# Kernel optimization log

Hardware: AMD Instinct MI355X
Metric: run time of the kernel (lower is better)

## Reference

```python
import jax, jax.numpy as jnp
import numpy as np

# --- MLA config (matches init_kwargs) ---
DIM = 2048
H = 16
KV_RANK = 512
Q_RANK = 1536
ROPE = 64          # qk_rope_head_dim (even)
NOPE = 128         # qk_nope_head_dim
VD = 128           # v_head_dim
THETA = 500000.0
EPS = 1e-6
B, T = 1, 2048
QK_HEAD = NOPE + ROPE  # logits use nope + rope dims


def _rmsnorm(x, w):
    # x float32; RMS over last dim, no mean subtraction
    rms = jax.lax.rsqrt(jnp.mean(x * x, axis=-1, keepdims=True) + EPS)
    return (x * rms) * w


def _rope_tables(t):
    inv_freq = 1.0 / (THETA ** (jnp.arange(0, ROPE, 2, dtype=jnp.float32) / ROPE))  # (ROPE/2,)
    pos = jnp.arange(t, dtype=jnp.float32)
    angles = jnp.outer(pos, inv_freq)  # (T, ROPE/2)
    return jnp.cos(angles), jnp.sin(angles)


def _apply_rope(x, cos, sin):
    # x: (B, T, Hx, D) with adjacent-pair rotation; cos/sin: (T, D/2)
    b, t, h, d = x.shape
    xp = x.reshape(b, t, h, d // 2, 2)
    even, odd = xp[..., 0], xp[..., 1]
    c = cos.reshape(1, t, 1, d // 2)
    s = sin.reshape(1, t, 1, d // 2)
    out = jnp.stack((even * c - odd * s, odd * c + even * s), axis=-1)
    return out.reshape(b, t, h, d)


def setup_inputs() -> dict:
    key = jax.random.key(0)
    ks = jax.random.split(key, 7)
    s = 0.02
    x = jax.random.normal(ks[0], (B, T, DIM), dtype=jnp.float32)
    w_q_down = jax.random.normal(ks[1], (Q_RANK, DIM), dtype=jnp.float32) * s
    q_norm_w = jnp.ones((Q_RANK,), dtype=jnp.float32)
    w_q_up = jax.random.normal(ks[2], (H * (NOPE + ROPE), Q_RANK), dtype=jnp.float32) * s
    w_kv_down = jax.random.normal(ks[3], (KV_RANK + ROPE, DIM), dtype=jnp.float32) * s
    kv_norm_w = jnp.ones((KV_RANK,), dtype=jnp.float32)
    w_kv_up = jax.random.normal(ks[4], (H * (NOPE + VD), KV_RANK), dtype=jnp.float32) * s
    w_o = jax.random.normal(ks[5], (DIM, H * VD), dtype=jnp.float32) * s
    return {"x": x, "w_q_down": w_q_down, "q_norm_w": q_norm_w, "w_q_up": w_q_up,
            "w_kv_down": w_kv_down, "kv_norm_w": kv_norm_w, "w_kv_up": w_kv_up, "w_o": w_o}


def reference(x, w_q_down, q_norm_w, w_q_up, w_kv_down, kv_norm_w, w_kv_up, w_o):
    b, t, _ = x.shape
    # Query path: down-proj -> RMSNorm -> up-proj, split nope/rope
    c_q = _rmsnorm(x @ w_q_down.T, q_norm_w)                       # (B,T,Q_RANK)
    q = (c_q @ w_q_up.T).reshape(b, t, H, NOPE + ROPE)
    q_nope, q_rope = q[..., :NOPE], q[..., NOPE:]
    # KV path: down-proj -> split latent c_kv and shared rope key
    kv = x @ w_kv_down.T                                           # (B,T,KV_RANK+ROPE)
    c_kv = kv[..., :KV_RANK]
    k_rope_raw = kv[..., KV_RANK:].reshape(b, t, 1, ROPE)
    # RoPE (adjacent-pair), start_pos=0
    cos, sin = _rope_tables(t)
    q_rope = _apply_rope(q_rope, cos, sin)
    k_rope = _apply_rope(k_rope_raw, cos, sin)                     # (B,T,1,ROPE) shared head
    # Reconstruct k_nope and v from normalized latent
    kv_up = (_rmsnorm(c_kv, kv_norm_w) @ w_kv_up.T).reshape(b, t, H, NOPE + VD)
    k_nope, v = kv_up[..., :NOPE], kv_up[..., NOPE:]
    # Assemble full q/k (rope key broadcast across heads)
    q_full = jnp.concatenate((q_nope, q_rope), axis=-1)            # (B,T,H,QK_HEAD)
    k_full = jnp.concatenate((k_nope, jnp.broadcast_to(k_rope, (b, t, H, ROPE))), axis=-1)
    # Causal attention
    scale = 1.0 / np.sqrt(QK_HEAD)
    scores = jnp.einsum('bqhd,bkhd->bhqk', q_full, k_full) * scale  # (B,H,T,T)
    causal = jnp.tril(jnp.ones((t, t), dtype=bool))
    scores = jnp.where(causal[None, None], scores, -jnp.inf)
    attn = jax.nn.softmax(scores, axis=-1)
    out = jnp.einsum('bhqk,bkhd->bqhd', attn, v).reshape(b, t, H * VD)
    return out @ w_o.T                                             # (B,T,DIM)
```

## Files before the change

kernel.cpp:

```cpp
#include <hip/hip_runtime.h>
#include <hip/hip_bf16.h>

typedef short short8 __attribute__((ext_vector_type(8)));
typedef float f32x4 __attribute__((ext_vector_type(4)));

#define DIM 2048
#define NH 16
#define KV_RANK 512
#define Q_RANK 1536
#define ROPE_D 64
#define NOPE 128
#define VD 128
#define TT 2048
#define QKH 192
#define QD (NH * QKH)
#define KVUP_D (NH * (NOPE + VD))
#define WDN 2176

__device__ inline unsigned short f2bf(float f) {
  __hip_bfloat16 h = __float2bfloat16(f);
  union { __hip_bfloat16 h; unsigned short u; } cv; cv.h = h; return cv.u;
}
__device__ inline float bf2f(unsigned short u) {
  union { unsigned int i; float f; } cv; cv.i = ((unsigned int)u) << 16; return cv.f;
}
__device__ inline void gload_lds16(const void* g, void* l) {
  __builtin_amdgcn_global_load_lds(
      (const __attribute__((address_space(1))) void*)g,
      (__attribute__((address_space(3))) void*)l, 16, 0, 0);
}

__global__ __launch_bounds__(256) void convert_all(
    const float* __restrict__ x, const float* __restrict__ wqd,
    const float* __restrict__ wkvd, const float* __restrict__ wqu,
    const float* __restrict__ wkvu, const float* __restrict__ wo,
    unsigned short* __restrict__ xb, unsigned short* __restrict__ wdb,
    unsigned short* __restrict__ wqub, unsigned short* __restrict__ wkvub,
    unsigned short* __restrict__ wob) {
  int i = blockIdx.x * 256 + threadIdx.x;
  const int n0 = TT * DIM / 4;
  const int n1 = WDN * 2048 / 4;
  const int n2 = QD * Q_RANK / 4;
  const int n3 = KVUP_D * KV_RANK / 4;
  const int n4 = DIM * DIM / 4;
  float4 v;
  unsigned short* dst;
  if (i < n0) { v = reinterpret_cast<const float4*>(x)[i]; dst = xb; }
  else if ((i -= n0) < n1) {
    int row = i >> 9, c4 = i & 511;
    if (row < 1536)      v = reinterpret_cast<const float4*>(wqd)[row * 512 + c4];
    else if (row < 2112) v = reinterpret_cast<const float4*>(wkvd)[(row - 1536) * 512 + c4];
    else                 v = make_float4(0.f, 0.f, 0.f, 0.f);
    dst = wdb;
  }
  else if ((i -= n1) < n2) { v = reinterpret_cast<const float4*>(wqu)[i]; dst = wqub; }
  else if ((i -= n2) < n3) { v = reinterpret_cast<const float4*>(wkvu)[i]; dst = wkvub; }
  else if ((i -= n3) < n4) { v = reinterpret_cast<const float4*>(wo)[i]; dst = wob; }
  else return;
  ushort4 o;
  o.x = f2bf(v.x); o.y = f2bf(v.y); o.z = f2bf(v.z); o.w = f2bf(v.w);
  reinterpret_cast<ushort4*>(dst)[i] = o;
}

__device__ __forceinline__ void gemm_core(const unsigned short* __restrict__ A,
                                          const unsigned short* __restrict__ W,
                                          unsigned short* As, unsigned short* Bs,
                                          int K, int lda, int ldb,
                                          int bm, int bn, int tid,
                                          f32x4 (&acc)[4][4]) {
  const int lane = tid & 63, wave = tid >> 6;
  const int wm = (wave >> 1) * 64, wn = (wave & 1) * 64;
  const int fr = lane & 15, fg = lane >> 4;
  const int sr = lane >> 3, scb = (lane & 7) ^ sr;
  const int r0 = wave * 32;

  const unsigned short* Ag = A + (size_t)(bm + r0 + sr) * lda + scb * 8;
  const unsigned short* Wg = W + (size_t)(bn + r0 + sr) * ldb + scb * 8;
  const int nt = K >> 6;

#pragma unroll
  for (int i = 0; i < 4; ++i) {
    gload_lds16(Ag + (size_t)(i * 8) * lda, As + r0 * 64 + i * 512);
    gload_lds16(Wg + (size_t)(i * 8) * ldb, Bs + r0 * 64 + i * 512);
  }
  int cur = 0;
  for (int t = 0; t < nt; ++t) {
    if (t + 1 < nt) {
      const int nb = cur ^ 1;
      const int ko = (t + 1) * 64;
#pragma unroll
      for (int i = 0; i < 4; ++i) {
        gload_lds16(Ag + ko + (size_t)(i * 8) * lda, As + nb * 8192 + r0 * 64 + i * 512);
        gload_lds16(Wg + ko + (size_t)(i * 8) * ldb, Bs + nb * 8192 + r0 * 64 + i * 512);
      }
      asm volatile("s_waitcnt vmcnt(8)" ::: "memory");
    } else {
      asm volatile("s_waitcnt vmcnt(0)" ::: "memory");
    }
    __builtin_amdgcn_s_barrier();
    asm volatile("" ::: "memory");
    const unsigned short* Ac = As + cur * 8192;
    const unsigned short* Bc = Bs + cur * 8192;
    __builtin_amdgcn_s_setprio(1);
#pragma unroll
    for (int kk = 0; kk < 2; ++kk) {
      short8 a[4], b[4];
#pragma unroll
      for (int i = 0; i < 4; ++i) {
        int ra = wm + i * 16 + fr;
        a[i] = *reinterpret_cast<const short8*>(&Ac[ra * 64 + (((kk * 4 + fg) ^ (ra & 7)) * 8)]);
        int rb = wn + i * 16 + fr;
        b[i] = *reinterpret_cast<const short8*>(&Bc[rb * 64 + (((kk * 4 + fg) ^ (rb & 7)) * 8)]);
      }
#pragma unroll
      for (int i = 0; i < 4; ++i)
#pragma unroll
        for (int j = 0; j < 4; ++j)
          acc[i][j] = __builtin_amdgcn_mfma_f32_16x16x32_bf16(a[i], b[j], acc[i][j], 0, 0, 0);
    }
    __builtin_amdgcn_s_setprio(0);
    asm volatile("" ::: "memory");
    __builtin_amdgcn_s_barrier();
    cur ^= 1;
  }
}

__global__ __launch_bounds__(256) void gemm_fast(const unsigned short* __restrict__ A,
                                                 const unsigned short* __restrict__ W,
                                                 float* __restrict__ Cf,
                                                 unsigned short* __restrict__ Cb,
                                                 int K, int lda, int ldb, int ldc) {
  __shared__ __align__(16) unsigned short As[2 * 128 * 64];
  __shared__ __align__(16) unsigned short Bs[2 * 128 * 64];
  const int tid = threadIdx.x;
  const int bm = blockIdx.y * 128, bn = blockIdx.x * 128;
  const int lane = tid & 63, wave = tid >> 6;
  const int wm = (wave >> 1) * 64, wn = (wave & 1) * 64;
  const int fr = lane & 15, fg = lane >> 4;

  f32x4 acc[4][4] = {};
  gemm_core(A, W, As, Bs, K, lda, ldb, bm, bn, tid, acc);

  if (Cb) {
#pragma unroll
    for (int i = 0; i < 4; ++i) {
      int row0 = bm + wm + i * 16 + fg * 4;
#pragma unroll
      for (int j = 0; j < 4; ++j) {
        int col = bn + wn + j * 16 + fr;
#pragma unroll
        for (int r = 0; r < 4; ++r)
          Cb[(size_t)(row0 + r) * ldc + col] = f2bf(acc[i][j][r]);
      }
    }
  } else {
#pragma unroll
    for (int i = 0; i < 4; ++i) {
      int row0 = bm + wm + i * 16 + fg * 4;
#pragma unroll
      for (int j = 0; j < 4; ++j) {
        int col = bn + wn + j * 16 + fr;
#pragma unroll
        for (int r = 0; r < 4; ++r)
          Cf[(size_t)(row0 + r) * ldc + col] = acc[i][j][r];
      }
    }
  }
}

__global__ __launch_bounds__(256) void gemm_dual(
    const unsigned short* __restrict__ A1, const unsigned short* __restrict__ W1,
    unsigned short* __restrict__ C1,
    const unsigned short* __restrict__ A2, const unsigned short* __restrict__ W2,
    unsigned short* __restrict__ kbuf, unsigned short* __restrict__ vt) {
  __shared__ __align__(16) unsigned short As[2 * 128 * 64];
  __shared__ __align__(16) unsigned short Bs[2 * 128 * 64];
  const int tid = threadIdx.x;
  const int bx = blockIdx.x;
  const unsigned short *A, *W;
  int K, lda, bm, bn;
  const bool isq = (bx < 384);
  if (isq) {
    A = A1; W = W1; K = Q_RANK; lda = Q_RANK;
    bn = (bx % 24) * 128; bm = (bx / 24) * 128;
  } else {
    int b2 = bx - 384;
    A = A2; W = W2; K = KV_RANK; lda = KV_RANK;
    bn = (b2 & 31) * 128; bm = (b2 >> 5) * 128;
  }
  const int lane = tid & 63, wave = tid >> 6;
  const int wm = (wave >> 1) * 64, wn = (wave & 1) * 64;
  const int fr = lane & 15, fg = lane >> 4;

  f32x4 acc[4][4] = {};
  gemm_core(A, W, As, Bs, K, lda, lda, bm, bn, tid, acc);

  if (isq) {
#pragma unroll
    for (int i = 0; i < 4; ++i) {
      int row0 = bm + wm + i * 16 + fg * 4;
#pragma unroll
      for (int j = 0; j < 4; ++j) {
        int col = bn + wn + j * 16 + fr;
#pragma unroll
        for (int r = 0; r < 4; ++r)
          C1[(size_t)(row0 + r) * QD + col] = f2bf(acc[i][j][r]);
      }
    }
  } else {
#pragma unroll
    for (int i = 0; i < 4; ++i) {
      int row0 = bm + wm + i * 16 + fg * 4;
#pragma unroll
      for (int j = 0; j < 4; ++j) {
        int col = bn + wn + j * 16 + fr;
        int hh = col >> 8, cc = col & 255;
        if (cc < 128) {
#pragma unroll
          for (int r = 0; r < 4; ++r)
            kbuf[((size_t)hh * TT + row0 + r) * QKH + cc] = f2bf(acc[i][j][r]);
        } else {
          ushort4 w4;
          w4.x = f2bf(acc[i][j][0]); w4.y = f2bf(acc[i][j][1]);
          w4.z = f2bf(acc[i][j][2]); w4.w = f2bf(acc[i][j][3]);
          *reinterpret_cast<ushort4*>(vt + (size_t)(hh * VD + cc - 128) * TT + row0) = w4;
        }
      }
    }
  }
}

__global__ __launch_bounds__(256) void rmsnorm_bf16(const unsigned short* __restrict__ in,
                                                    int instride, int inoff,
                                                    const float* __restrict__ w,
                                                    unsigned short* __restrict__ out,
                                                    int outstride, int cols) {
  const int row = blockIdx.x, tid = threadIdx.x;
  const unsigned short* x = in + (size_t)row * instride + inoff;
  const int nch = cols >> 3;
  float ss = 0.f;
  for (int cb = tid; cb < nch; cb += 256) {
    short8 v = *reinterpret_cast<const short8*>(x + cb * 8);
#pragma unroll
    for (int e = 0; e < 8; ++e) { float f = bf2f((unsigned short)v[e]); ss += f * f; }
  }
  __shared__ float red[256];
  red[tid] = ss; __syncthreads();
  for (int off = 128; off > 0; off >>= 1) {
    if (tid < off) red[tid] += red[tid + off];
    __syncthreads();
  }
  float r = rsqrtf(red[0] / (float)cols + 1e-6f);
  for (int cb = tid; cb < nch; cb += 256) {
    short8 v = *reinterpret_cast<const short8*>(x + cb * 8);
    ushort4 o0, o1;
    o0.x = f2bf(bf2f((unsigned short)v[0]) * r * w[cb * 8 + 0]);
    o0.y = f2bf(bf2f((unsigned short)v[1]) * r * w[cb * 8 + 1]);
    o0.z = f2bf(bf2f((unsigned short)v[2]) * r * w[cb * 8 + 2]);
    o0.w = f2bf(bf2f((unsigned short)v[3]) * r * w[cb * 8 + 3]);
    o1.x = f2bf(bf2f((unsigned short)v[4]) * r * w[cb * 8 + 4]);
    o1.y = f2bf(bf2f((unsigned short)v[5]) * r * w[cb * 8 + 5]);
    o1.z = f2bf(bf2f((unsigned short)v[6]) * r * w[cb * 8 + 6]);
    o1.w = f2bf(bf2f((unsigned short)v[7]) * r * w[cb * 8 + 7]);
    *reinterpret_cast<ushort4*>(out + (size_t)row * outstride + cb * 8) = o0;
    *reinterpret_cast<ushort4*>(out + (size_t)row * outstride + cb * 8 + 4) = o1;
  }
}

__global__ __launch_bounds__(256) void rope_kernel(unsigned short* __restrict__ qb,
                                                   const unsigned short* __restrict__ cqkv,
                                                   unsigned short* __restrict__ kbuf) {
  const int t = blockIdx.x, tid = threadIdx.x;
  unsigned short* qrow = qb + (size_t)t * QD;
  for (int p = tid; p < NH * 32 + 32; p += 256) {
    int j = (p < NH * 32) ? (p & 31) : (p - NH * 32);
    float inv = powf(500000.0f, -(float)(2 * j) * (1.0f / 64.0f));
    float ang = (float)t * inv;
    float sv, cv;
    sincosf(ang, &sv, &cv);
    if (p < NH * 32) {
      int h = p >> 5;
      unsigned short* b = qrow + h * QKH + NOPE + 2 * j;
      float e = bf2f(b[0]), o = bf2f(b[1]);
      b[0] = f2bf(e * cv - o * sv);
      b[1] = f2bf(o * cv + e * sv);
    } else {
      const unsigned short* b = cqkv + (size_t)t * WDN + 2048 + 2 * j;
      float e = bf2f(b[0]), o = bf2f(b[1]);
      unsigned short re = f2bf(e * cv - o * sv);
      unsigned short ro = f2bf(o * cv + e * sv);
#pragma unroll
      for (int hh = 0; hh < NH; ++hh) {
        kbuf[((size_t)hh * TT + t) * QKH + NOPE + 2 * j]     = re;
        kbuf[((size_t)hh * TT + t) * QKH + NOPE + 2 * j + 1] = ro;
      }
    }
  }
}

__global__ __launch_bounds__(256, 2) void attn_part(
    const unsigned short* __restrict__ qb,
    const unsigned short* __restrict__ kbuf,
    const unsigned short* __restrict__ vtb,
    unsigned short* __restrict__ Opart,
    float* __restrict__ ml)
{
  const int b = blockIdx.x;
  const int h = b & 15;
  const int w = b >> 4;
  int qt, c;
  if (w < 16)      { qt = 15 - (w >> 2); c = w & 3; }
  else if (w < 28) { int v = w - 16; qt = 11 - v / 3; c = v % 3; }
  else if (w < 36) { int v = w - 28; qt = 7 - ((w - 28) >> 1); c = v & 1; }
  else             { qt = 3 - (w - 36); c = 0; }
  const int t0 = qt * 128;
  const int ktlo = c * 8;
  const int kthi = min(c * 8 + 8, 2 * qt + 2);
  const int tid = threadIdx.x;
  const int lane = tid & 63, wv = tid >> 6;
  const int fr = lane & 15, fg = lane >> 4;

  __shared__ __align__(16) unsigned short KVl[2560 * 8];
  __shared__ __align__(16) unsigned short Ps[4][16 * 64];
  unsigned short* Kl = KVl;
  unsigned short* Vt = KVl + 12288;

  short8 qf[2][6];
#pragma unroll
  for (int s = 0; s < 2; ++s) {
    const unsigned short* qrow = qb + (size_t)(t0 + wv * 32 + s * 16 + fr) * QD + h * QKH;
#pragma unroll
    for (int kc = 0; kc < 6; ++kc)
      qf[s][kc] = *reinterpret_cast<const short8*>(qrow + kc * 32 + fg * 8);
  }

  f32x4 o[2][8] = {};
  float m2[2] = {-1e30f, -1e30f};
  float l2[2] = {0.f, 0.f};
  const float scale = 0.0721687836487032f;
  const unsigned short* kb = kbuf + (size_t)h * TT * QKH;
  const unsigned short* vb = vtb + (size_t)h * VD * TT;

  for (int kt = ktlo; kt < kthi; ++kt) {
    const int kt0 = kt * 64;
#pragma unroll
    for (int i = 0; i < 6; ++i) {
      int u = tid + i * 256;
      int row = u / 24, cb = u - (u / 24) * 24;
      int cbs = cb ^ (row & 7);
      gload_lds16(kb + (size_t)(kt0 + row) * QKH + cbs * 8, Kl + u * 8);
    }
#pragma unroll
    for (int i = 0; i < 4; ++i) {
      int u = tid + i * 256;
      int d = u >> 3, cb = u & 7;
      int cbs = cb ^ (d & 7);
      gload_lds16(vb + (size_t)d * TT + kt0 + cbs * 8, Vt + u * 8);
    }
    asm volatile("s_waitcnt vmcnt(0)" ::: "memory");
    __syncthreads();

    f32x4 sA[2][4] = {};
    __builtin_amdgcn_s_setprio(1);
#pragma unroll
    for (int kc = 0; kc < 6; ++kc) {
#pragma unroll
      for (int kr = 0; kr < 4; ++kr) {
        int row = kr * 16 + fr;
        short8 kf = *reinterpret_cast<const short8*>(
            &Kl[row * QKH + (((kc * 4 + fg) ^ (row & 7)) * 8)]);
        sA[0][kr] = __builtin_amdgcn_mfma_f32_16x16x32_bf16(kf, qf[0][kc], sA[0][kr], 0, 0, 0);
        sA[1][kr] = __builtin_amdgcn_mfma_f32_16x16x32_bf16(kf, qf[1][kc], sA[1][kr], 0, 0, 0);
      }
    }
    __builtin_amdgcn_s_setprio(0);

    const bool diag = (kt0 + 64 > t0);
#pragma unroll
    for (int s = 0; s < 2; ++s) {
      const int qg = t0 + wv * 32 + s * 16 + fr;
      float mx = -1e30f;
#pragma unroll
      for (int kr = 0; kr < 4; ++kr)
#pragma unroll
        for (int r = 0; r < 4; ++r) {
          float svv = sA[s][kr][r] * scale;
          if (diag && (kt0 + kr * 16 + fg * 4 + r) > qg) svv = -1e30f;
          sA[s][kr][r] = svv;
          mx = fmaxf(mx, svv);
        }
      mx = fmaxf(mx, __shfl_xor(mx, 16));
      mx = fmaxf(mx, __shfl_xor(mx, 32));
      float mn = fmaxf(m2[s], mx);
      float corr = __expf(m2[s] - mn);
      m2[s] = mn;
      float ssum = 0.f;
#pragma unroll
      for (int kr = 0; kr < 4; ++kr) {
        ushort4 pk;
        float p0 = __expf(sA[s][kr][0] - mn);
        float p1 = __expf(sA[s][kr][1] - mn);
        float p2 = __expf(sA[s][kr][2] - mn);
        float p3 = __expf(sA[s][kr][3] - mn);
        ssum += p0 + p1 + p2 + p3;
        pk.x = f2bf(p0); pk.y = f2bf(p1); pk.z = f2bf(p2); pk.w = f2bf(p3);
        *reinterpret_cast<ushort4*>(
            &Ps[wv][fr * 64 + (((kr * 2 + (fg >> 1)) ^ (fr & 7)) * 8) + (fg & 1) * 4]) = pk;
      }
      ssum += __shfl_xor(ssum, 16);
      ssum += __shfl_xor(ssum, 32);
      l2[s] = l2[s] * corr + ssum;
      if (__any(corr != 1.0f)) {
        float c0 = __shfl(corr, fg * 4 + 0);
        float c1 = __shfl(corr, fg * 4 + 1);
        float c2 = __shfl(corr, fg * 4 + 2);
        float c3 = __shfl(corr, fg * 4 + 3);
#pragma unroll
        for (int dj = 0; dj < 8; ++dj) {
          o[s][dj][0] *= c0; o[s][dj][1] *= c1;
          o[s][dj][2] *= c2; o[s][dj][3] *= c3;
        }
      }
      __builtin_amdgcn_s_setprio(1);
#pragma unroll
      for (int kk = 0; kk < 2; ++kk) {
        short8 pa = *reinterpret_cast<const short8*>(
            &Ps[wv][fr * 64 + (((kk * 4 + fg) ^ (fr & 7)) * 8)]);
#pragma unroll
        for (int dj = 0; dj < 8; ++dj) {
          int dv = dj * 16 + fr;
          short8 bv = *reinterpret_cast<const short8*>(
              &Vt[dv * 64 + (((kk * 4 + fg) ^ (dv & 7)) * 8)]);
          o[s][dj] = __builtin_amdgcn_mfma_f32_16x16x32_bf16(pa, bv, o[s][dj], 0, 0, 0);
        }
      }
      __builtin_amdgcn_s_setprio(0);
    }
    __syncthreads();
  }

  const int slot = (h * 16 + qt) * 4 + c;
#pragma unroll
  for (int s = 0; s < 2; ++s) {
#pragma unroll
    for (int r = 0; r < 4; ++r) {
      int row = wv * 32 + s * 16 + fg * 4 + r;
      unsigned short* orow = Opart + ((size_t)slot * 128 + row) * 128;
#pragma unroll
      for (int dj = 0; dj < 8; ++dj)
        orow[dj * 16 + fr] = f2bf(o[s][dj][r]);
    }
    if (fg == 0) {
      int row = wv * 32 + s * 16 + fr;
      ml[((size_t)slot * 128 + row) * 2]     = m2[s];
      ml[((size_t)slot * 128 + row) * 2 + 1] = l2[s];
    }
  }
}

__global__ __launch_bounds__(256) void attn_combine(
    const unsigned short* __restrict__ Opart, const float* __restrict__ ml,
    unsigned short* __restrict__ out) {
  const int bid = blockIdx.x;
  const int h = bid >> 5;
  const int qt = (bid >> 1) & 15;
  const int rh = bid & 1;
  const int nch = qt / 4 + 1;
  const int tid = threadIdx.x;
  const int row = rh * 64 + (tid >> 2), dg = tid & 3;
  const int base = (h * 16 + qt) * 4;
  float mm[4], ll[4];
  float M = -1e30f;
#pragma unroll
  for (int cc = 0; cc < 4; ++cc) {
    if (cc < nch) {
      mm[cc] = ml[((size_t)(base + cc) * 128 + row) * 2];
      ll[cc] = ml[((size_t)(base + cc) * 128 + row) * 2 + 1];
      M = fmaxf(M, mm[cc]);
    } else { mm[cc] = -1e30f; ll[cc] = 0.f; }
  }
  float L = 0.f;
#pragma unroll
  for (int cc = 0; cc < 4; ++cc) {
    mm[cc] = __expf(mm[cc] - M);
    L += ll[cc] * mm[cc];
  }
  float acc[32] = {};
#pragma unroll
  for (int cc = 0; cc < 4; ++cc) {
    if (cc < nch) {
      const unsigned short* op = Opart + ((size_t)(base + cc) * 128 + row) * 128 + dg * 32;
      float sc = mm[cc];
#pragma unroll
      for (int e8 = 0; e8 < 4; ++e8) {
        short8 v = *reinterpret_cast<const short8*>(op + e8 * 8);
#pragma unroll
        for (int e = 0; e < 8; ++e) acc[e8 * 8 + e] += bf2f((unsigned short)v[e]) * sc;
      }
    }
  }
  float linv = 1.0f / L;
  unsigned short* dst = out + (size_t)(qt * 128 + row) * DIM + h * VD + dg * 32;
#pragma unroll
  for (int e4 = 0; e4 < 8; ++e4) {
    ushort4 w4;
    w4.x = f2bf(acc[e4 * 4 + 0] * linv);
    w4.y = f2bf(acc[e4 * 4 + 1] * linv);
    w4.z = f2bf(acc[e4 * 4 + 2] * linv);
    w4.w = f2bf(acc[e4 * 4 + 3] * linv);
    *reinterpret_cast<ushort4*>(dst + e4 * 4) = w4;
  }
}

extern "C" void kernel_launch(void* const* d_in, const int* in_sizes, int n_in,
                              void* d_out, int out_size, void* d_ws, size_t ws_size,
                              hipStream_t stream) {
  const float* x        = (const float*)d_in[0];
  const float* w_q_down = (const float*)d_in[1];
  const float* q_norm_w = (const float*)d_in[2];
  const float* w_q_up   = (const float*)d_in[3];
  const float* w_kv_down= (const float*)d_in[4];
  const float* kv_norm_w= (const float*)d_in[5];
  const float* w_kv_up  = (const float*)d_in[6];
  const float* w_o      = (const float*)d_in[7];
  float* outp = (float*)d_out;

  char* ws = (char*)d_ws;
  size_t off = 0;
  auto alloc = [&](size_t bytes) {
    void* p = ws + off;
    off += (bytes + 255) & ~(size_t)255;
    return p;
  };
  unsigned short* x_bf     = (unsigned short*)alloc((size_t)TT * DIM * 2);
  unsigned short* wdown_bf = (unsigned short*)alloc((size_t)WDN * DIM * 2);
  unsigned short* wqu_bf   = (unsigned short*)alloc((size_t)QD * Q_RANK * 2);
  unsigned short* wkvu_bf  = (unsigned short*)alloc((size_t)KVUP_D * KV_RANK * 2);
  unsigned short* wo_bf    = (unsigned short*)alloc((size_t)DIM * DIM * 2);
  unsigned short* cqkv_bf  = (unsigned short*)alloc((size_t)TT * WDN * 2);
  unsigned short* cq_bf    = (unsigned short*)alloc((size_t)TT * Q_RANK * 2);
  unsigned short* ckv_bf   = (unsigned short*)alloc((size_t)TT * KV_RANK * 2);
  unsigned short* qb_bf    = (unsigned short*)alloc((size_t)TT * QD * 2);
  unsigned short* kbuf     = (unsigned short*)alloc((size_t)NH * TT * QKH * 2);
  unsigned short* vtb      = (unsigned short*)alloc((size_t)NH * VD * TT * 2);
  unsigned short* Opart    = (unsigned short*)alloc((size_t)1024 * 128 * 128 * 2);
  float*          mlbuf    = (float*)alloc((size_t)1024 * 128 * 2 * 4);
  unsigned short* attn_bf  = x_bf;

  {
    int total = TT * DIM / 4 + WDN * 2048 / 4 + QD * Q_RANK / 4 +
                KVUP_D * KV_RANK / 4 + DIM * DIM / 4;
    convert_all<<<dim3((total + 255) / 256), dim3(256), 0, stream>>>(
        x, w_q_down, w_kv_down, w_q_up, w_kv_up, w_o,
        x_bf, wdown_bf, wqu_bf, wkvu_bf, wo_bf);
  }

  dim3 blk(256);
  gemm_fast<<<dim3(WDN / 128, TT / 128), blk, 0, stream>>>(
      x_bf, wdown_bf, nullptr, cqkv_bf, DIM, DIM, DIM, WDN);
  rmsnorm_bf16<<<dim3(TT), blk, 0, stream>>>(cqkv_bf, WDN, 0, q_norm_w, cq_bf, Q_RANK, Q_RANK);
  rmsnorm_bf16<<<dim3(TT), blk, 0, stream>>>(cqkv_bf, WDN, Q_RANK, kv_norm_w, ckv_bf, KV_RANK, KV_RANK);
  gemm_dual<<<dim3(896), blk, 0, stream>>>(cq_bf, wqu_bf, qb_bf,
                                           ckv_bf, wkvu_bf, kbuf, vtb);
  rope_kernel<<<dim3(TT), blk, 0, stream>>>(qb_bf, cqkv_bf, kbuf);
  attn_part<<<dim3(640), blk, 0, stream>>>(qb_bf, kbuf, vtb, Opart, mlbuf);
  attn_combine<<<dim3(512), blk, 0, stream>>>(Opart, mlbuf, attn_bf);
  gemm_fast<<<dim3(DIM / 128, TT / 128), blk, 0, stream>>>(
      attn_bf, wo_bf, outp, nullptr, DIM, DIM, DIM, DIM);
}
```

Baseline: 217.9 us.

## Double-buffer K/V tiles in attention with smaller 32-key steps

Splits the K/V tile into 32-key chunks and double-buffers them in LDS, so the global-to-LDS load of the next chunk is issued before computing on the current one, with partial vmcnt waits. The PV product now shares each V fragment across both query subtiles, and the P staging buffer uses a padded layout instead of an XOR swizzle. The aim is to hide global load latency behind MFMA work, at the cost of more loop iterations, more barriers per key, and a possible LDS bank-conflict change from the padded V layout.

After: 227.9 us. 4.6% more time.

```diff
diff --git a/kernel.cpp b/kernel.cpp
--- a/kernel.cpp
+++ b/kernel.cpp
@@ -311,19 +311,38 @@
   int qt, c;
   if (w < 16)      { qt = 15 - (w >> 2); c = w & 3; }
   else if (w < 28) { int v = w - 16; qt = 11 - v / 3; c = v % 3; }
-  else if (w < 36) { int v = w - 28; qt = 7 - ((w - 28) >> 1); c = v & 1; }
+  else if (w < 36) { qt = 7 - ((w - 28) >> 1); c = (w - 28) & 1; }
   else             { qt = 3 - (w - 36); c = 0; }
   const int t0 = qt * 128;
-  const int ktlo = c * 8;
-  const int kthi = min(c * 8 + 8, 2 * qt + 2);
+  const int ktlo = c * 16;
+  const int kthi = min(c * 16 + 16, 4 * qt + 4);
   const int tid = threadIdx.x;
   const int lane = tid & 63, wv = tid >> 6;
   const int fr = lane & 15, fg = lane >> 4;
 
-  __shared__ __align__(16) unsigned short KVl[2560 * 8];
-  __shared__ __align__(16) unsigned short Ps[4][16 * 64];
-  unsigned short* Kl = KVl;
-  unsigned short* Vt = KVl + 12288;
+  __shared__ __align__(16) unsigned short KV[2][12288];
+  __shared__ __align__(16) unsigned short Ps[4][2][16 * 40];
+
+  const unsigned short* kb = kbuf + (size_t)h * TT * QKH;
+  const unsigned short* vb = vtb + (size_t)h * VD * TT;
+
+  auto STAGE = [&](int bi, int kt) {
+    const int kt0s = kt * 32;
+#pragma unroll
+    for (int i = 0; i < 3; ++i) {
+      int u = tid + i * 256;
+      int row = u / 24, cb = u - (u / 24) * 24;
+      gload_lds16(kb + (size_t)(kt0s + row) * QKH + ((cb ^ (row & 7)) * 8),
+                  &KV[bi][u * 8]);
+    }
+#pragma unroll
+    for (int i = 0; i < 3; ++i) {
+      int u = tid + i * 256;
+      int d = u / 6, cb = u - (u / 6) * 6;
+      int cbs = (cb < 4) ? cb : 0;
+      gload_lds16(vb + (size_t)d * TT + kt0s + cbs * 8, &KV[bi][6144 + u * 8]);
+    }
+  };
 
   short8 qf[2][6];
 #pragma unroll
@@ -333,55 +352,51 @@
     for (int kc = 0; kc < 6; ++kc)
       qf[s][kc] = *reinterpret_cast<const short8*>(qrow + kc * 32 + fg * 8);
   }
+  asm volatile("s_waitcnt vmcnt(0)" ::: "memory");
+
+  STAGE(0, ktlo);
 
   f32x4 o[2][8] = {};
   float m2[2] = {-1e30f, -1e30f};
   float l2[2] = {0.f, 0.f};
   const float scale = 0.0721687836487032f;
-  const unsigned short* kb = kbuf + (size_t)h * TT * QKH;
-  const unsigned short* vb = vtb + (size_t)h * VD * TT;
-
+
+  int buf = 0;
   for (int kt = ktlo; kt < kthi; ++kt) {
-    const int kt0 = kt * 64;
-#pragma unroll
-    for (int i = 0; i < 6; ++i) {
-      int u = tid + i * 256;
-      int row = u / 24, cb = u - (u / 24) * 24;
-      int cbs = cb ^ (row & 7);
-      gload_lds16(kb + (size_t)(kt0 + row) * QKH + cbs * 8, Kl + u * 8);
-    }
-#pragma unroll
-    for (int i = 0; i < 4; ++i) {
-      int u = tid + i * 256;
-      int d = u >> 3, cb = u & 7;
-      int cbs = cb ^ (d & 7);
-      gload_lds16(vb + (size_t)d * TT + kt0 + cbs * 8, Vt + u * 8);
-    }
-    asm volatile("s_waitcnt vmcnt(0)" ::: "memory");
-    __syncthreads();
-
-    f32x4 sA[2][4] = {};
+    const int kt0 = kt * 32;
+    if (kt + 1 < kthi) {
+      STAGE(buf ^ 1, kt + 1);
+      asm volatile("s_waitcnt vmcnt(6)" ::: "memory");
+    } else {
+      asm volatile("s_waitcnt vmcnt(0)" ::: "memory");
+    }
+    __builtin_amdgcn_s_barrier();
+    asm volatile("" ::: "memory");
+    const unsigned short* Kb = KV[buf];
+    const unsigned short* Vt = KV[buf] + 6144;
+
+    f32x4 sA[2][2] = {};
     __builtin_amdgcn_s_setprio(1);
 #pragma unroll
     for (int kc = 0; kc < 6; ++kc) {
 #pragma unroll
-      for (int kr = 0; kr < 4; ++kr) {
+      for (int kr = 0; kr < 2; ++kr) {
         int row = kr * 16 + fr;
         short8 kf = *reinterpret_cast<const short8*>(
-            &Kl[row * QKH + (((kc * 4 + fg) ^ (row & 7)) * 8)]);
+            &Kb[row * QKH + (((kc * 4 + fg) ^ (row & 7)) * 8)]);
         sA[0][kr] = __builtin_amdgcn_mfma_f32_16x16x32_bf16(kf, qf[0][kc], sA[0][kr], 0, 0, 0);
         sA[1][kr] = __builtin_amdgcn_mfma_f32_16x16x32_bf16(kf, qf[1][kc], sA[1][kr], 0, 0, 0);
       }
     }
     __builtin_amdgcn_s_setprio(0);
 
-    const bool diag = (kt0 + 64 > t0);
+    const bool diag = (kt0 + 32 > t0);
 #pragma unroll
     for (int s = 0; s < 2; ++s) {
       const int qg = t0 + wv * 32 + s * 16 + fr;
       float mx = -1e30f;
 #pragma unroll
-      for (int kr = 0; kr < 4; ++kr)
+      for (int kr = 0; kr < 2; ++kr)
 #pragma unroll
         for (int r = 0; r < 4; ++r) {
           float svv = sA[s][kr][r] * scale;
@@ -396,16 +411,15 @@
       m2[s] = mn;
       float ssum = 0.f;
 #pragma unroll
-      for (int kr = 0; kr < 4; ++kr) {
-        ushort4 pk;
+      for (int kr = 0; kr < 2; ++kr) {
         float p0 = __expf(sA[s][kr][0] - mn);
         float p1 = __expf(sA[s][kr][1] - mn);
         float p2 = __expf(sA[s][kr][2] - mn);
         float p3 = __expf(sA[s][kr][3] - mn);
         ssum += p0 + p1 + p2 + p3;
+        ushort4 pk;
         pk.x = f2bf(p0); pk.y = f2bf(p1); pk.z = f2bf(p2); pk.w = f2bf(p3);
-        *reinterpret_cast<ushort4*>(
-            &Ps[wv][fr * 64 + (((kr * 2 + (fg >> 1)) ^ (fr & 7)) * 8) + (fg & 1) * 4]) = pk;
+        *reinterpret_cast<ushort4*>(&Ps[wv][s][fr * 40 + kr * 16 + fg * 4]) = pk;
       }
       ssum += __shfl_xor(ssum, 16);
       ssum += __shfl_xor(ssum, 32);
@@ -421,22 +435,22 @@
           o[s][dj][2] *= c2; o[s][dj][3] *= c3;
         }
       }
-      __builtin_amdgcn_s_setprio(1);
-#pragma unroll
-      for (int kk = 0; kk < 2; ++kk) {
-        short8 pa = *reinterpret_cast<const short8*>(
-            &Ps[wv][fr * 64 + (((kk * 4 + fg) ^ (fr & 7)) * 8)]);
-#pragma unroll
-        for (int dj = 0; dj < 8; ++dj) {
-          int dv = dj * 16 + fr;
-          short8 bv = *reinterpret_cast<const short8*>(
-              &Vt[dv * 64 + (((kk * 4 + fg) ^ (dv & 7)) * 8)]);
-          o[s][dj] = __builtin_amdgcn_mfma_f32_16x16x32_bf16(pa, bv, o[s][dj], 0, 0, 0);
-        }
-      }
-      __builtin_amdgcn_s_setprio(0);
-    }
-    __syncthreads();
+    }
+
+    short8 pa0 = *reinterpret_cast<const short8*>(&Ps[wv][0][fr * 40 + fg * 8]);
+    short8 pa1 = *reinterpret_cast<const short8*>(&Ps[wv][1][fr * 40 + fg * 8]);
+    __builtin_amdgcn_s_setprio(1);
+#pragma unroll
+    for (int dj = 0; dj < 8; ++dj) {
+      int dv = dj * 16 + fr;
+      short8 bv = *reinterpret_cast<const short8*>(&Vt[dv * 48 + fg * 8]);
+      o[0][dj] = __builtin_amdgcn_mfma_f32_16x16x32_bf16(pa0, bv, o[0][dj], 0, 0, 0);
+      o[1][dj] = __builtin_amdgcn_mfma_f32_16x16x32_bf16(pa1, bv, o[1][dj], 0, 0, 0);
+    }
+    __builtin_amdgcn_s_setprio(0);
+    asm volatile("" ::: "memory");
+    __builtin_amdgcn_s_barrier();
+    buf ^= 1;
   }
 
   const int slot = (h * 16 + qt) * 4 + c;
```

## Fuse fp32 weight conversion into GEMM B-tile loads and swizzle block order

Applied to the files above, without the earlier changes.

Removes the standalone conversion pass over all weights. GEMMs now read fp32 weights directly into registers, convert them to bf16, and write them to swizzled LDS, overlapping the B loads with the MFMA compute of the previous tile. Block indices are remapped with a stride-8 interleave, presumably to improve L2 locality across dies, and the kernels request 2 blocks per CU. The cost is twice the global bytes per weight load inside the GEMM, plus register pressure from holding fp32 data. Weights are also re-read and re-converted by every M-tile row.

Measured after the change: 359.4 us. +65.0%, slower.

```diff
diff --git a/kernel.cpp b/kernel.cpp
--- a/kernel.cpp
+++ b/kernel.cpp
@@ -16,6 +16,7 @@
 #define QD (NH * QKH)
 #define KVUP_D (NH * (NOPE + VD))
 #define WDN 2176
+#define KVD_ROWS 576
 
 __device__ inline unsigned short f2bf(float f) {
   __hip_bfloat16 h = __float2bfloat16(f);
@@ -30,44 +31,23 @@
       (__attribute__((address_space(3))) void*)l, 16, 0, 0);
 }
 
-__global__ __launch_bounds__(256) void convert_all(
-    const float* __restrict__ x, const float* __restrict__ wqd,
-    const float* __restrict__ wkvd, const float* __restrict__ wqu,
-    const float* __restrict__ wkvu, const float* __restrict__ wo,
-    unsigned short* __restrict__ xb, unsigned short* __restrict__ wdb,
-    unsigned short* __restrict__ wqub, unsigned short* __restrict__ wkvub,
-    unsigned short* __restrict__ wob) {
+__global__ __launch_bounds__(256) void convert_x(const float* __restrict__ in,
+                                                 unsigned short* __restrict__ out,
+                                                 int n4) {
   int i = blockIdx.x * 256 + threadIdx.x;
-  const int n0 = TT * DIM / 4;
-  const int n1 = WDN * 2048 / 4;
-  const int n2 = QD * Q_RANK / 4;
-  const int n3 = KVUP_D * KV_RANK / 4;
-  const int n4 = DIM * DIM / 4;
-  float4 v;
-  unsigned short* dst;
-  if (i < n0) { v = reinterpret_cast<const float4*>(x)[i]; dst = xb; }
-  else if ((i -= n0) < n1) {
-    int row = i >> 9, c4 = i & 511;
-    if (row < 1536)      v = reinterpret_cast<const float4*>(wqd)[row * 512 + c4];
-    else if (row < 2112) v = reinterpret_cast<const float4*>(wkvd)[(row - 1536) * 512 + c4];
-    else                 v = make_float4(0.f, 0.f, 0.f, 0.f);
-    dst = wdb;
-  }
-  else if ((i -= n1) < n2) { v = reinterpret_cast<const float4*>(wqu)[i]; dst = wqub; }
-  else if ((i -= n2) < n3) { v = reinterpret_cast<const float4*>(wkvu)[i]; dst = wkvub; }
-  else if ((i -= n3) < n4) { v = reinterpret_cast<const float4*>(wo)[i]; dst = wob; }
-  else return;
+  if (i >= n4) return;
+  float4 v = reinterpret_cast<const float4*>(in)[i];
   ushort4 o;
   o.x = f2bf(v.x); o.y = f2bf(v.y); o.z = f2bf(v.z); o.w = f2bf(v.w);
-  reinterpret_cast<ushort4*>(dst)[i] = o;
-}
-
-__device__ __forceinline__ void gemm_core(const unsigned short* __restrict__ A,
-                                          const unsigned short* __restrict__ W,
-                                          unsigned short* As, unsigned short* Bs,
-                                          int K, int lda, int ldb,
-                                          int bm, int bn, int tid,
-                                          f32x4 (&acc)[4][4]) {
+  reinterpret_cast<ushort4*>(out)[i] = o;
+}
+
+__device__ __forceinline__ void gemm_core_w32(
+    const unsigned short* __restrict__ A,
+    const float* __restrict__ W1, const float* __restrict__ W2,
+    int wsplit, int wvalid, int ldw,
+    unsigned short* As, unsigned short* Bs,
+    int K, int lda, int bm, int bn, int tid, f32x4 (&acc)[4][4]) {
   const int lane = tid & 63, wave = tid >> 6;
   const int wm = (wave >> 1) * 64, wn = (wave & 1) * 64;
   const int fr = lane & 15, fg = lane >> 4;
@@ -75,29 +55,60 @@
   const int r0 = wave * 32;
 
   const unsigned short* Ag = A + (size_t)(bm + r0 + sr) * lda + scb * 8;
-  const unsigned short* Wg = W + (size_t)(bn + r0 + sr) * ldb + scb * 8;
+
+  const int rloc = lane >> 1, half = lane & 1;
+  const int grow = bn + r0 + rloc;
+  const bool wz = (grow >= wvalid);
+  const float* wrow;
+  if (grow < wsplit)  wrow = W1 + (size_t)grow * ldw;
+  else if (!wz)       wrow = W2 + (size_t)(grow - wsplit) * ldw;
+  else                wrow = W2;
+  wrow += half * 32;
+  const int brow = r0 + rloc;
+  const int bso = brow * 64;
+
   const int nt = K >> 6;
-
-#pragma unroll
-  for (int i = 0; i < 4; ++i) {
-    gload_lds16(Ag + (size_t)(i * 8) * lda, As + r0 * 64 + i * 512);
-    gload_lds16(Wg + (size_t)(i * 8) * ldb, Bs + r0 * 64 + i * 512);
-  }
+  float4 br[8];
+
+#define ISSUE_B(k0)                                                      \
+  { _Pragma("unroll")                                                    \
+    for (int j = 0; j < 8; ++j)                                          \
+      br[j] = *reinterpret_cast<const float4*>(wrow + (k0) + j * 4); }
+#define ISSUE_A(nb, k0)                                                  \
+  { _Pragma("unroll")                                                    \
+    for (int i = 0; i < 4; ++i)                                          \
+      gload_lds16(Ag + (k0) + (size_t)(i * 8) * lda,                     \
+                  As + (nb) * 8192 + r0 * 64 + i * 512); }
+#define WRITE_B(nb)                                                      \
+  { _Pragma("unroll")                                                    \
+    for (int i = 0; i < 4; ++i) {                                        \
+      float4 f0 = wz ? make_float4(0.f,0.f,0.f,0.f) : br[2*i];           \
+      float4 f1 = wz ? make_float4(0.f,0.f,0.f,0.f) : br[2*i+1];         \
+      short8 v;                                                          \
+      v[0] = (short)f2bf(f0.x); v[1] = (short)f2bf(f0.y);                \
+      v[2] = (short)f2bf(f0.z); v[3] = (short)f2bf(f0.w);                \
+      v[4] = (short)f2bf(f1.x); v[5] = (short)f2bf(f1.y);                \
+      v[6] = (short)f2bf(f1.z); v[7] = (short)f2bf(f1.w);                \
+      int cb = half * 4 + i;                                             \
+      *reinterpret_cast<short8*>(                                        \
+          &Bs[(nb) * 8192 + bso + ((cb ^ (brow & 7)) * 8)]) = v;         \
+    } }
+
+  ISSUE_B(0);
+  ISSUE_A(0, 0);
+  asm volatile("s_waitcnt vmcnt(4)" ::: "memory");
+  WRITE_B(0);
+  asm volatile("s_waitcnt vmcnt(0)" ::: "memory");
+  __builtin_amdgcn_s_barrier();
+
   int cur = 0;
   for (int t = 0; t < nt; ++t) {
+    const int nb = cur ^ 1;
     if (t + 1 < nt) {
-      const int nb = cur ^ 1;
       const int ko = (t + 1) * 64;
-#pragma unroll
-      for (int i = 0; i < 4; ++i) {
-        gload_lds16(Ag + ko + (size_t)(i * 8) * lda, As + nb * 8192 + r0 * 64 + i * 512);
-        gload_lds16(Wg + ko + (size_t)(i * 8) * ldb, Bs + nb * 8192 + r0 * 64 + i * 512);
-      }
-      asm volatile("s_waitcnt vmcnt(8)" ::: "memory");
-    } else {
-      asm volatile("s_waitcnt vmcnt(0)" ::: "memory");
-    }
-    __builtin_amdgcn_s_barrier();
+      ISSUE_B(ko);
+      ISSUE_A(nb, ko);
+    }
     asm volatile("" ::: "memory");
     const unsigned short* Ac = As + cur * 8192;
     const unsigned short* Bc = Bs + cur * 8192;
@@ -119,27 +130,40 @@
           acc[i][j] = __builtin_amdgcn_mfma_f32_16x16x32_bf16(a[i], b[j], acc[i][j], 0, 0, 0);
     }
     __builtin_amdgcn_s_setprio(0);
-    asm volatile("" ::: "memory");
+    if (t + 1 < nt) {
+      asm volatile("s_waitcnt vmcnt(4)" ::: "memory");
+      WRITE_B(nb);
+    }
+    asm volatile("s_waitcnt vmcnt(0)" ::: "memory");
     __builtin_amdgcn_s_barrier();
     cur ^= 1;
   }
-}
-
-__global__ __launch_bounds__(256) void gemm_fast(const unsigned short* __restrict__ A,
-                                                 const unsigned short* __restrict__ W,
-                                                 float* __restrict__ Cf,
-                                                 unsigned short* __restrict__ Cb,
-                                                 int K, int lda, int ldb, int ldc) {
+#undef ISSUE_B
+#undef ISSUE_A
+#undef WRITE_B
+}
+
+__global__ __launch_bounds__(256, 2) void gemm_w32(
+    const unsigned short* __restrict__ A,
+    const float* __restrict__ W1, const float* __restrict__ W2,
+    int wsplit, int wvalid, int ldw,
+    float* __restrict__ Cf, unsigned short* __restrict__ Cb,
+    int K, int lda, int ldc) {
   __shared__ __align__(16) unsigned short As[2 * 128 * 64];
   __shared__ __align__(16) unsigned short Bs[2 * 128 * 64];
   const int tid = threadIdx.x;
-  const int bm = blockIdx.y * 128, bn = blockIdx.x * 128;
+  const int gy = gridDim.y;
+  const int w = blockIdx.y * gridDim.x + blockIdx.x;
+  const int nwg = gridDim.x * gridDim.y;
+  const int s = (w & 7) * (nwg >> 3) + (w >> 3);
+  const int bxs = s / gy, bys = s - bxs * gy;
+  const int bm = bys * 128, bn = bxs * 128;
   const int lane = tid & 63, wave = tid >> 6;
   const int wm = (wave >> 1) * 64, wn = (wave & 1) * 64;
   const int fr = lane & 15, fg = lane >> 4;
 
   f32x4 acc[4][4] = {};
-  gemm_core(A, W, As, Bs, K, lda, ldb, bm, bn, tid, acc);
+  gemm_core_w32(A, W1, W2, wsplit, wvalid, ldw, As, Bs, K, lda, bm, bn, tid, acc);
 
   if (Cb) {
 #pragma unroll
@@ -168,24 +192,27 @@
   }
 }
 
-__global__ __launch_bounds__(256) void gemm_dual(
-    const unsigned short* __restrict__ A1, const unsigned short* __restrict__ W1,
+__global__ __launch_bounds__(256, 2) void gemm_dual_w32(
+    const unsigned short* __restrict__ A1, const float* __restrict__ W1f,
     unsigned short* __restrict__ C1,
-    const unsigned short* __restrict__ A2, const unsigned short* __restrict__ W2,
+    const unsigned short* __restrict__ A2, const float* __restrict__ W2f,
     unsigned short* __restrict__ kbuf, unsigned short* __restrict__ vt) {
   __shared__ __align__(16) unsigned short As[2 * 128 * 64];
   __shared__ __align__(16) unsigned short Bs[2 * 128 * 64];
   const int tid = threadIdx.x;
-  const int bx = blockIdx.x;
-  const unsigned short *A, *W;
+  const int w = blockIdx.x;
+  const int nwg = gridDim.x;
+  const int s = (w & 7) * (nwg >> 3) + (w >> 3);
+  const unsigned short* A;
+  const float* Wf;
   int K, lda, bm, bn;
-  const bool isq = (bx < 384);
+  const bool isq = (s < 384);
   if (isq) {
-    A = A1; W = W1; K = Q_RANK; lda = Q_RANK;
-    bn = (bx % 24) * 128; bm = (bx / 24) * 128;
+    A = A1; Wf = W1f; K = Q_RANK; lda = Q_RANK;
+    bn = (s % 24) * 128; bm = (s / 24) * 128;
   } else {
-    int b2 = bx - 384;
-    A = A2; W = W2; K = KV_RANK; lda = KV_RANK;
+    int b2 = s - 384;
+    A = A2; Wf = W2f; K = KV_RANK; lda = KV_RANK;
     bn = (b2 & 31) * 128; bm = (b2 >> 5) * 128;
   }
   const int lane = tid & 63, wave = tid >> 6;
@@ -193,7 +220,7 @@
   const int fr = lane & 15, fg = lane >> 4;
 
   f32x4 acc[4][4] = {};
-  gemm_core(A, W, As, Bs, K, lda, lda, bm, bn, tid, acc);
+  gemm_core_w32(A, Wf, Wf, 0x7fffffff, 0x7fffffff, lda, As, Bs, K, lda, bm, bn, tid, acc);
 
   if (isq) {
 #pragma unroll
@@ -311,7 +338,7 @@
   int qt, c;
   if (w < 16)      { qt = 15 - (w >> 2); c = w & 3; }
   else if (w < 28) { int v = w - 16; qt = 11 - v / 3; c = v % 3; }
-  else if (w < 36) { int v = w - 28; qt = 7 - ((w - 28) >> 1); c = v & 1; }
+  else if (w < 36) { qt = 7 - ((w - 28) >> 1); c = (w - 28) & 1; }
   else             { qt = 3 - (w - 36); c = 0; }
   const int t0 = qt * 128;
   const int ktlo = c * 8;
@@ -533,10 +560,6 @@
     return p;
   };
   unsigned short* x_bf     = (unsigned short*)alloc((size_t)TT * DIM * 2);
-  unsigned short* wdown_bf = (unsigned short*)alloc((size_t)WDN * DIM * 2);
-  unsigned short* wqu_bf   = (unsigned short*)alloc((size_t)QD * Q_RANK * 2);
-  unsigned short* wkvu_bf  = (unsigned short*)alloc((size_t)KVUP_D * KV_RANK * 2);
-  unsigned short* wo_bf    = (unsigned short*)alloc((size_t)DIM * DIM * 2);
   unsigned short* cqkv_bf  = (unsigned short*)alloc((size_t)TT * WDN * 2);
   unsigned short* cq_bf    = (unsigned short*)alloc((size_t)TT * Q_RANK * 2);
   unsigned short* ckv_bf   = (unsigned short*)alloc((size_t)TT * KV_RANK * 2);
@@ -547,24 +570,20 @@
   float*          mlbuf    = (float*)alloc((size_t)1024 * 128 * 2 * 4);
   unsigned short* attn_bf  = x_bf;
 
-  {
-    int total = TT * DIM / 4 + WDN * 2048 / 4 + QD * Q_RANK / 4 +
-                KVUP_D * KV_RANK / 4 + DIM * DIM / 4;
-    convert_all<<<dim3((total + 255) / 256), dim3(256), 0, stream>>>(
-        x, w_q_down, w_kv_down, w_q_up, w_kv_up, w_o,
-        x_bf, wdown_bf, wqu_bf, wkvu_bf, wo_bf);
-  }
-
   dim3 blk(256);
-  gemm_fast<<<dim3(WDN / 128, TT / 128), blk, 0, stream>>>(
-      x_bf, wdown_bf, nullptr, cqkv_bf, DIM, DIM, DIM, WDN);
+  convert_x<<<dim3((TT * DIM / 4 + 255) / 256), blk, 0, stream>>>(x, x_bf, TT * DIM / 4);
+
+  gemm_w32<<<dim3(WDN / 128, TT / 128), blk, 0, stream>>>(
+      x_bf, w_q_down, w_kv_down, Q_RANK, Q_RANK + KVD_ROWS, DIM,
+      nullptr, cqkv_bf, DIM, DIM, WDN);
   rmsnorm_bf16<<<dim3(TT), blk, 0, stream>>>(cqkv_bf, WDN, 0, q_norm_w, cq_bf, Q_RANK, Q_RANK);
   rmsnorm_bf16<<<dim3(TT), blk, 0, stream>>>(cqkv_bf, WDN, Q_RANK, kv_norm_w, ckv_bf, KV_RANK, KV_RANK);
-  gemm_dual<<<dim3(896), blk, 0, stream>>>(cq_bf, wqu_bf, qb_bf,
-                                           ckv_bf, wkvu_bf, kbuf, vtb);
+  gemm_dual_w32<<<dim3(896), blk, 0, stream>>>(cq_bf, w_q_up, qb_bf,
+                                               ckv_bf, w_kv_up, kbuf, vtb);
   rope_kernel<<<dim3(TT), blk, 0, stream>>>(qb_bf, cqkv_bf, kbuf);
   attn_part<<<dim3(640), blk, 0, stream>>>(qb_bf, kbuf, vtb, Opart, mlbuf);
   attn_combine<<<dim3(512), blk, 0, stream>>>(Opart, mlbuf, attn_bf);
-  gemm_fast<<<dim3(DIM / 128, TT / 128), blk, 0, stream>>>(
-      attn_bf, wo_bf, outp, nullptr, DIM, DIM, DIM, DIM);
-}
+  gemm_w32<<<dim3(DIM / 128, TT / 128), blk, 0, stream>>>(
+      attn_bf, w_o, w_o, 0x7fffffff, 0x7fffffff, DIM,
+      outp, nullptr, DIM, DIM, DIM);
+}
```
